# Optimization experiments

Hardware: AMD Instinct MI355X
Metric: run time of the kernel (lower is better)

The kernel has to match this reference:

```python
import jax, jax.numpy as jnp
import numpy as np

DIM = 768
HEADS = 12
HIDDEN = 4 * DIM
EPS = 1e-5


def _layer_norm(x, g, b):
    mu = jnp.mean(x, axis=-1, keepdims=True)
    var = jnp.mean(jnp.square(x - mu), axis=-1, keepdims=True)
    return (x - mu) * jax.lax.rsqrt(var + EPS) * g + b


def setup_inputs() -> dict:
    key = jax.random.key(0)
    ks = jax.random.split(key, 10)
    B, N, C = 16, 1024, DIM
    s = lambda fan: 1.0 / np.sqrt(fan)
    return {
        "x": jax.random.normal(ks[0], (B, N, C), dtype=jnp.float32),
        "ln1_g": jnp.ones((C,), jnp.float32),
        "ln1_b": jnp.zeros((C,), jnp.float32),
        "qkv_w": jax.random.normal(ks[1], (C, 3 * C), jnp.float32) * s(C),
        "qkv_b": jnp.zeros((3 * C,), jnp.float32),
        "proj_w": jax.random.normal(ks[2], (C, C), jnp.float32) * s(C),
        "proj_b": jnp.zeros((C,), jnp.float32),
        "ln2_g": jnp.ones((C,), jnp.float32),
        "ln2_b": jnp.zeros((C,), jnp.float32),
        "fc1_w": jax.random.normal(ks[3], (C, HIDDEN), jnp.float32) * s(C),
        "fc1_b": jnp.zeros((HIDDEN,), jnp.float32),
        "fc2_w": jax.random.normal(ks[4], (HIDDEN, C), jnp.float32) * s(HIDDEN),
        "fc2_b": jnp.zeros((C,), jnp.float32),
    }


def reference(x, ln1_g, ln1_b, qkv_w, qkv_b, proj_w, proj_b,
              ln2_g, ln2_b, fc1_w, fc1_b, fc2_w, fc2_b):
    B, N, C = x.shape
    Hd = C // HEADS
    scale = Hd ** -0.5

    # --- attention branch (pre-norm) ---
    h = _layer_norm(x, ln1_g, ln1_b)
    qkv = h @ qkv_w + qkv_b                       # [B,N,3C]
    qkv = qkv.reshape(B, N, 3, HEADS, Hd).transpose(2, 0, 3, 1, 4)
    q, k, v = qkv[0], qkv[1], qkv[2]              # [B,H,N,Hd]
    attn = jnp.einsum("bhqd,bhkd->bhqk", q, k) * scale
    attn = jax.nn.softmax(attn, axis=-1)
    o = jnp.einsum("bhqk,bhkd->bhqd", attn, v)    # [B,H,N,Hd]
    o = o.transpose(0, 2, 1, 3).reshape(B, N, C)
    x = x + (o @ proj_w + proj_b)

    # --- MLP branch (pre-norm) ---
    h = _layer_norm(x, ln2_g, ln2_b)
    h = jax.nn.gelu(h @ fc1_w + fc1_b, approximate=False)
    x = x + (h @ fc2_w + fc2_b)
    return x
```

## Files before the change

kernel.cpp:

```cpp
#include <hip/hip_runtime.h>

typedef __bf16 bf16x8 __attribute__((ext_vector_type(8)));
typedef __bf16 bf16x4 __attribute__((ext_vector_type(4)));
typedef float f32x4 __attribute__((ext_vector_type(4)));
typedef float f32x16 __attribute__((ext_vector_type(16)));

#define MFMA16(a,b,c) __builtin_amdgcn_mfma_f32_16x16x32_bf16((a),(b),(c),0,0,0)
#define MFMA32(a,b,c) __builtin_amdgcn_mfma_f32_32x32x16_bf16((a),(b),(c),0,0,0)
#define EXP2R(x) __builtin_amdgcn_exp2f(x)

#define BB   16
#define SEQ  1024
#define CD   768
#define NHD  12
#define HDD  64
#define HID  3072
#define MT   (BB*SEQ)

__device__ __forceinline__ void gload16(const void* g, void* l) {
    __builtin_amdgcn_global_load_lds(
        (const __attribute__((address_space(1))) void*)g,
        (__attribute__((address_space(3))) void*)l, 16, 0, 0);
}

__device__ __forceinline__ unsigned pk2(float lo, float hi) {
    unsigned short a = __builtin_bit_cast(unsigned short, (__bf16)lo);
    unsigned short b = __builtin_bit_cast(unsigned short, (__bf16)hi);
    return (unsigned)a | ((unsigned)b << 16);
}

__device__ __forceinline__ float fast_gelu(float x) {
    float u = x * x * x;
    float y = fmaf(0.044715f, u, x);
    float e = EXP2R(-2.3022083f * y);
    return x * __builtin_amdgcn_rcpf(1.0f + e);
}

__global__ __launch_bounds__(256)
void transpose_w(const float* __restrict__ W, __bf16* __restrict__ WT, int R, int C)
{
    __shared__ float t[32][33];
    int tc = C >> 5;
    int bid = blockIdx.x;
    int br = bid / tc, bc = bid % tc;
    int x = threadIdx.x & 31, y = threadIdx.x >> 5;
#pragma unroll
    for (int i = 0; i < 4; ++i)
        t[y + 8*i][x] = W[(size_t)(br*32 + y + 8*i)*C + bc*32 + x];
    __syncthreads();
#pragma unroll
    for (int i = 0; i < 4; ++i)
        WT[(size_t)(bc*32 + y + 8*i)*R + br*32 + x] = (__bf16)t[x][y + 8*i];
}

__global__ __launch_bounds__(256)
void ln_kernel(const float* __restrict__ xin, const float* __restrict__ g,
               const float* __restrict__ bb, __bf16* out)
{
    int row = blockIdx.x * 4 + (threadIdx.x >> 6);
    int lane = threadIdx.x & 63;
    const float* xr = xin + (size_t)row * CD + lane * 4;
    float4 v0 = *(const float4*)(xr);
    float4 v1 = *(const float4*)(xr + 256);
    float4 v2 = *(const float4*)(xr + 512);
    float s = v0.x+v0.y+v0.z+v0.w + v1.x+v1.y+v1.z+v1.w + v2.x+v2.y+v2.z+v2.w;
#pragma unroll
    for (int off = 1; off < 64; off <<= 1) s += __shfl_xor(s, off);
    float mu = s * (1.0f/768.0f);
    float q =
        (v0.x-mu)*(v0.x-mu)+(v0.y-mu)*(v0.y-mu)+(v0.z-mu)*(v0.z-mu)+(v0.w-mu)*(v0.w-mu)+
        (v1.x-mu)*(v1.x-mu)+(v1.y-mu)*(v1.y-mu)+(v1.z-mu)*(v1.z-mu)+(v1.w-mu)*(v1.w-mu)+
        (v2.x-mu)*(v2.x-mu)+(v2.y-mu)*(v2.y-mu)+(v2.z-mu)*(v2.z-mu)+(v2.w-mu)*(v2.w-mu);
#pragma unroll
    for (int off = 1; off < 64; off <<= 1) q += __shfl_xor(q, off);
    float rstd = rsqrtf(q * (1.0f/768.0f) + 1e-5f);

    __bf16* orow = out + (size_t)row * CD + lane * 4;
#pragma unroll
    for (int p = 0; p < 3; ++p) {
        float4 xv = (p == 0) ? v0 : (p == 1) ? v1 : v2;
        float4 gv = *(const float4*)(g  + p*256 + lane*4);
        float4 bv = *(const float4*)(bb + p*256 + lane*4);
        bf16x4 ov;
        ov[0] = (__bf16)((xv.x-mu)*rstd*gv.x + bv.x);
        ov[1] = (__bf16)((xv.y-mu)*rstd*gv.y + bv.y);
        ov[2] = (__bf16)((xv.z-mu)*rstd*gv.z + bv.z);
        ov[3] = (__bf16)((xv.w-mu)*rstd*gv.w + bv.w);
        *(bf16x4*)(orow + p*256) = ov;
    }
}

template<int EPI>
__global__ __launch_bounds__(256)
void gemm_bt(const __bf16* __restrict__ A, const __bf16* __restrict__ BT,
             const float* __restrict__ bias,
             const float* res, float* outf,
             __bf16* __restrict__ outb,
             __bf16* __restrict__ qb, __bf16* __restrict__ kb, __bf16* __restrict__ vb,
             int M, int N, int K)
{
    __shared__ alignas(16) __bf16 lsA[2][128*64];
    __shared__ alignas(16) __bf16 lsB[2][128*64];

    int nbn = N >> 7;
    int nwg = (M >> 7) * nbn;
    int bid = (int)blockIdx.x;
    int cpx = nwg >> 3;
    int sw = (bid & 7) * cpx + (bid >> 3);
    int bm = sw / nbn, bn = sw % nbn;
    int row0 = bm << 7, col0 = bn << 7;

    int tid = threadIdx.x;
    int lane = tid & 63, w = tid >> 6;
    int wr = w >> 1, wc = w & 1;
    int lr = lane & 15, lg = lane >> 4;

    f32x4 acc[4][4] = {};
    int sbase = w * 4096 + lane * 16;
    int swz = (lr & 7) << 4;

    auto stage = [&](int buf, int ktE) {
#pragma unroll
        for (int i = 0; i < 4; ++i) {
            int s = sbase + (i << 10);
            int r = s >> 7;
            int ch = ((s >> 4) & 7) ^ (r & 7);
            gload16(A  + (size_t)(row0 + r)*K + (ktE + ch*8),
                    (char*)lsA + buf*16384 + (w*4 + i)*1024);
            gload16(BT + (size_t)(col0 + r)*K + (ktE + ch*8),
                    (char*)lsB + buf*16384 + (w*4 + i)*1024);
        }
    };

    int nkt = K >> 6;
    stage(0, 0);
    __syncthreads();
    int cur = 0;

    for (int kt = 0; kt < nkt; ++kt) {
        if (kt + 1 < nkt) stage(cur ^ 1, (kt + 1) << 6);

        const char* lA = (const char*)lsA + cur*16384;
        const char* lB = (const char*)lsB + cur*16384;
#pragma unroll
        for (int ks = 0; ks < 2; ++ks) {
            int cb = (ks*64 + lg*16) ^ swz;
            bf16x8 af[4], bfv[4];
#pragma unroll
            for (int m = 0; m < 4; ++m) {
                af[m]  = *(const bf16x8*)(lA + (wr*64 + m*16 + lr)*128 + cb);
                bfv[m] = *(const bf16x8*)(lB + (wc*64 + m*16 + lr)*128 + cb);
            }
#pragma unroll
            for (int m = 0; m < 4; ++m)
#pragma unroll
                for (int n = 0; n < 4; ++n)
                    acc[m][n] = MFMA16(af[m], bfv[n], acc[m][n]);
        }
        __syncthreads();
        cur ^= 1;
    }

    int rbase = row0 + wr*64 + lg*4;
    int cbase = col0 + wc*64 + lr;
#pragma unroll
    for (int n = 0; n < 4; ++n) {
        int col = cbase + n*16;
        float bv = bias[col];
        if constexpr (EPI == 0) {
            int which = col / CD;
            int c2 = col - which * CD;
            int head = c2 >> 6, d = c2 & 63;
#pragma unroll
            for (int m = 0; m < 4; ++m) {
                int r0 = rbase + m*16;
                int b = r0 >> 10, nn = r0 & 1023;
                if (which == 2) {
                    bf16x4 pv;
#pragma unroll
                    for (int j = 0; j < 4; ++j) pv[j] = (__bf16)(acc[m][n][j] + bv);
                    *(bf16x4*)&vb[(((size_t)b*NHD + head)*HDD + d)*SEQ + nn] = pv;
                } else {
                    __bf16* dst = (which == 0) ? qb : kb;
#pragma unroll
                    for (int j = 0; j < 4; ++j)
                        dst[(((size_t)b*NHD + head)*SEQ + nn + j)*HDD + d] =
                            (__bf16)(acc[m][n][j] + bv);
                }
            }
        } else {
#pragma unroll
            for (int m = 0; m < 4; ++m) {
                int rr = rbase + m*16;
#pragma unroll
                for (int j = 0; j < 4; ++j) {
                    float val = acc[m][n][j] + bv;
                    int r = rr + j;
                    if constexpr (EPI == 1) {
                        outf[(size_t)r*N + col] = res[(size_t)r*N + col] + val;
                    } else {
                        outb[(size_t)r*N + col] = (__bf16)fast_gelu(val);
                    }
                }
            }
        }
    }
}

__global__ __launch_bounds__(256)
void attn_kernel(const __bf16* __restrict__ q, const __bf16* __restrict__ k,
                 const __bf16* __restrict__ vT, __bf16* __restrict__ o)
{
    __shared__ alignas(16) __bf16 kls[2][64*64];
    __shared__ alignas(16) __bf16 vls[2][64*64];

    int bid = blockIdx.x;
    int u = bid >> 3, x = bid & 7;
    int bh = x*24 + (u >> 3);
    int qt = u & 7;
    int b = bh / NHD, hh = bh % NHD;
    int tid = threadIdx.x, lane = tid & 63, w = tid >> 6;
    int lq = lane & 31, h = lane >> 5;

    int qg = qt*128 + w*32 + lq;
    const __bf16* qp = q + ((size_t)bh*SEQ + qg)*HDD + h*8;
    bf16x8 qf[4];
#pragma unroll
    for (int s = 0; s < 4; ++s) qf[s] = *(const bf16x8*)(qp + s*16);

    const __bf16* kbase = k  + (size_t)bh*SEQ*HDD;
    const __bf16* vbase = vT + (size_t)bh*HDD*SEQ;

    int srow0 = tid >> 3;
    int scol0 = ((tid & 7) ^ (srow0 & 7)) * 8;
    int srow1 = srow0 + 32;

    auto stage = [&](int buf, int kv) {
        char* kl = (char*)kls + buf*8192 + w*1024;
        char* vl = (char*)vls + buf*8192 + w*1024;
        gload16(kbase + (size_t)(kv + srow0)*HDD + scol0, kl);
        gload16(kbase + (size_t)(kv + srow1)*HDD + scol0, kl + 4096);
        gload16(vbase + (size_t)srow0*SEQ + kv + scol0, vl);
        gload16(vbase + (size_t)srow1*SEQ + kv + scol0, vl + 4096);
    };

    const float SCL2 = 0.125f * 1.44269504f;
    const float NB   = -12.0f * SCL2;
    float lrun = 0.f;
    f32x16 oa0 = {}, oa1 = {};

    stage(0, 0);
    __syncthreads();
    int cur = 0;
    int rswz = (lq & 7) << 4;

    for (int kt = 0; kt < SEQ/64; ++kt) {
        if (kt + 1 < SEQ/64) stage(cur ^ 1, (kt + 1)*64);

        const char* kc = (const char*)kls + cur*8192;
        const char* vc = (const char*)vls + cur*8192;

        bf16x8 ka0[4], ka1[4];
#pragma unroll
        for (int s = 0; s < 4; ++s) {
            int bc = (h*16 + s*32) ^ rswz;
            ka0[s] = *(const bf16x8*)(kc + lq*128 + bc);
            ka1[s] = *(const bf16x8*)(kc + (lq + 32)*128 + bc);
        }
        bf16x8 vf0[4], vf1[4];
#pragma unroll
        for (int g = 0; g < 4; ++g) {
            int bc = (h*16 + g*32) ^ rswz;
            vf0[g] = *(const bf16x8*)(vc + lq*128 + bc);
            vf1[g] = *(const bf16x8*)(vc + (lq + 32)*128 + bc);
        }

        f32x16 s0 = {}, s1 = {};
        __builtin_amdgcn_s_setprio(1);
#pragma unroll
        for (int s = 0; s < 4; ++s) {
            s0 = MFMA32(ka0[s], qf[s], s0);
            s1 = MFMA32(ka1[s], qf[s], s1);
        }
        __builtin_amdgcn_s_setprio(0);

#pragma unroll
        for (int i = 0; i < 16; ++i) s0[i] = EXP2R(fmaf(s0[i], SCL2, NB));
#pragma unroll
        for (int i = 0; i < 16; ++i) s1[i] = EXP2R(fmaf(s1[i], SCL2, NB));
        float a8[8];
#pragma unroll
        for (int i = 0; i < 8; ++i)
            a8[i] = (s0[i] + s0[i + 8]) + (s1[i] + s1[i + 8]);
        float s4a = (a8[0] + a8[1]) + (a8[2] + a8[3]);
        float s4b = (a8[4] + a8[5]) + (a8[6] + a8[7]);
        lrun += s4a + s4b;

#pragma unroll
        for (int t = 0; t < 2; ++t) {
            const f32x16& sp = t ? s1 : s0;
            unsigned d0 = pk2(sp[ 0], sp[ 1]);
            unsigned d1 = pk2(sp[ 2], sp[ 3]);
            unsigned d2 = pk2(sp[ 4], sp[ 5]);
            unsigned d3 = pk2(sp[ 6], sp[ 7]);
            unsigned d4 = pk2(sp[ 8], sp[ 9]);
            unsigned d5 = pk2(sp[10], sp[11]);
            unsigned d6 = pk2(sp[12], sp[13]);
            unsigned d7 = pk2(sp[14], sp[15]);
            unsigned pd0 = __shfl_xor(d0, 32), pd1 = __shfl_xor(d1, 32);
            unsigned pd2 = __shfl_xor(d2, 32), pd3 = __shfl_xor(d3, 32);
            unsigned pd4 = __shfl_xor(d4, 32), pd5 = __shfl_xor(d5, 32);
            unsigned pd6 = __shfl_xor(d6, 32), pd7 = __shfl_xor(d7, 32);
            union { unsigned u[4]; bf16x8 v; } f0, f1;
            f0.u[0] = h ? pd2 : d0;
            f0.u[1] = h ? pd3 : d1;
            f0.u[2] = h ? d2 : pd0;
            f0.u[3] = h ? d3 : pd1;
            f1.u[0] = h ? pd6 : d4;
            f1.u[1] = h ? pd7 : d5;
            f1.u[2] = h ? d6 : pd4;
            f1.u[3] = h ? d7 : pd5;
            __builtin_amdgcn_s_setprio(1);
            oa0 = MFMA32(vf0[t*2 + 0], f0.v, oa0);
            oa1 = MFMA32(vf1[t*2 + 0], f0.v, oa1);
            oa0 = MFMA32(vf0[t*2 + 1], f1.v, oa0);
            oa1 = MFMA32(vf1[t*2 + 1], f1.v, oa1);
            __builtin_amdgcn_s_setprio(0);
        }

        __syncthreads();
        cur ^= 1;
    }

    lrun += __shfl_xor(lrun, 32);
    float inv = __builtin_amdgcn_rcpf(lrun);
    oa0 = oa0 * inv;
    oa1 = oa1 * inv;
    __bf16* orow = o + ((size_t)b*SEQ + qg)*CD + hh*HDD;
#pragma unroll
    for (int dt = 0; dt < 2; ++dt) {
        f32x16 oa = dt ? oa1 : oa0;
        unsigned d0 = pk2(oa[ 0], oa[ 1]);
        unsigned d1 = pk2(oa[ 2], oa[ 3]);
        unsigned d2 = pk2(oa[ 4], oa[ 5]);
        unsigned d3 = pk2(oa[ 6], oa[ 7]);
        unsigned d4 = pk2(oa[ 8], oa[ 9]);
        unsigned d5 = pk2(oa[10], oa[11]);
        unsigned d6 = pk2(oa[12], oa[13]);
        unsigned d7 = pk2(oa[14], oa[15]);
        unsigned pd0 = __shfl_xor(d0, 32), pd1 = __shfl_xor(d1, 32);
        unsigned pd2 = __shfl_xor(d2, 32), pd3 = __shfl_xor(d3, 32);
        unsigned pd4 = __shfl_xor(d4, 32), pd5 = __shfl_xor(d5, 32);
        unsigned pd6 = __shfl_xor(d6, 32), pd7 = __shfl_xor(d7, 32);
        union { unsigned u[4]; bf16x8 v; } g0, g1;
        g0.u[0] = h ? pd2 : d0;
        g0.u[1] = h ? pd3 : d1;
        g0.u[2] = h ? d2 : pd0;
        g0.u[3] = h ? d3 : pd1;
        g1.u[0] = h ? pd6 : d4;
        g1.u[1] = h ? pd7 : d5;
        g1.u[2] = h ? d6 : pd4;
        g1.u[3] = h ? d7 : pd5;
        *(bf16x8*)(orow + dt*32 +  0 + h*8) = g0.v;
        *(bf16x8*)(orow + dt*32 + 16 + h*8) = g1.v;
    }
}

extern "C" void kernel_launch(void* const* d_in, const int* in_sizes, int n_in,
                              void* d_out, int out_size, void* d_ws, size_t ws_size,
                              hipStream_t stream)
{
    const float* x     = (const float*)d_in[0];
    const float* ln1g  = (const float*)d_in[1];
    const float* ln1b  = (const float*)d_in[2];
    const float* qkvw  = (const float*)d_in[3];
    const float* qkvb  = (const float*)d_in[4];
    const float* projw = (const float*)d_in[5];
    const float* projb = (const float*)d_in[6];
    const float* ln2g  = (const float*)d_in[7];
    const float* ln2b  = (const float*)d_in[8];
    const float* fc1w  = (const float*)d_in[9];
    const float* fc1b  = (const float*)d_in[10];
    const float* fc2w  = (const float*)d_in[11];
    const float* fc2b  = (const float*)d_in[12];
    float* out = (float*)d_out;

    char* p = (char*)d_ws;
    auto alloc = [&](size_t bytes) { char* r = p; p += (bytes + 255) & ~(size_t)255; return r; };
    __bf16* wqkvT  = (__bf16*)alloc((size_t)3*CD*CD*2);
    __bf16* wprojT = (__bf16*)alloc((size_t)CD*CD*2);
    __bf16* wfc1T  = (__bf16*)alloc((size_t)HID*CD*2);
    __bf16* wfc2T  = (__bf16*)alloc((size_t)CD*HID*2);
    __bf16* hbuf   = (__bf16*)alloc((size_t)MT*CD*2);
    __bf16* qbuf   = (__bf16*)alloc((size_t)BB*NHD*SEQ*HDD*2);
    __bf16* kbuf   = (__bf16*)alloc((size_t)BB*NHD*SEQ*HDD*2);
    __bf16* vtbuf  = (__bf16*)alloc((size_t)BB*NHD*SEQ*HDD*2);
    (void)alloc((size_t)BB*NHD*SEQ*HDD*2);
    __bf16* hhbuf  = qbuf;

    transpose_w<<<(CD/32)*(3*CD/32), 256, 0, stream>>>(qkvw,  wqkvT, CD, 3*CD);
    transpose_w<<<(CD/32)*(CD/32),   256, 0, stream>>>(projw, wprojT, CD, CD);
    transpose_w<<<(CD/32)*(HID/32),  256, 0, stream>>>(fc1w,  wfc1T, CD, HID);
    transpose_w<<<(HID/32)*(CD/32),  256, 0, stream>>>(fc2w,  wfc2T, HID, CD);

    ln_kernel<<<MT/4, 256, 0, stream>>>(x, ln1g, ln1b, hbuf);

    gemm_bt<0><<<(MT/128)*(3*CD/128), 256, 0, stream>>>(
        hbuf, wqkvT, qkvb, nullptr, nullptr, nullptr, qbuf, kbuf, vtbuf, MT, 3*CD, CD);

    attn_kernel<<<BB*NHD*8, 256, 0, stream>>>(qbuf, kbuf, vtbuf, hbuf);

    gemm_bt<1><<<(MT/128)*(CD/128), 256, 0, stream>>>(
        hbuf, wprojT, projb, x, out, nullptr, nullptr, nullptr, nullptr, MT, CD, CD);

    ln_kernel<<<MT/4, 256, 0, stream>>>(out, ln2g, ln2b, hbuf);

    gemm_bt<2><<<(MT/128)*(HID/128), 256, 0, stream>>>(
        hbuf, wfc1T, fc1b, nullptr, nullptr, hhbuf, nullptr, nullptr, nullptr, MT, HID, CD);

    gemm_bt<1><<<(MT/128)*(CD/128), 256, 0, stream>>>(
        hhbuf, wfc2T, fc2b, out, out, nullptr, nullptr, nullptr, nullptr, MT, CD, HID);
}
```

Before: 463.5 us.

## Load GEMM B operand directly to registers and fuse prep kernels into one launch

The GEMM no longer stages the B (weight) tile through LDS. Each wave loads its B fragments straight from global memory into registers, which halves LDS use and allows a launch bound of 3 blocks per CU. The sync scheme becomes raw s_barrier with a manual vmcnt wait. Separately, the four weight transposes and the first layernorm are merged into one prep kernel launch to cut launch overhead. The risks are uncoalesced or redundant global B loads across waves, more register pressure, and fragile hand-written waitcnt counts.

```diff
diff --git a/kernel.cpp b/kernel.cpp
--- a/kernel.cpp
+++ b/kernel.cpp
@@ -8,6 +8,7 @@
 #define MFMA16(a,b,c) __builtin_amdgcn_mfma_f32_16x16x32_bf16((a),(b),(c),0,0,0)
 #define MFMA32(a,b,c) __builtin_amdgcn_mfma_f32_32x32x16_bf16((a),(b),(c),0,0,0)
 #define EXP2R(x) __builtin_amdgcn_exp2f(x)
+#define SBAR() asm volatile("s_barrier" ::: "memory")
 
 #define BB   16
 #define SEQ  1024
@@ -36,12 +37,11 @@
     return x * __builtin_amdgcn_rcpf(1.0f + e);
 }
 
-__global__ __launch_bounds__(256)
-void transpose_w(const float* __restrict__ W, __bf16* __restrict__ WT, int R, int C)
-{
-    __shared__ float t[32][33];
+__device__ __forceinline__ void transpose_body(
+    const float* __restrict__ W, __bf16* __restrict__ WT, int R, int C, int bid,
+    float (*t)[33])
+{
     int tc = C >> 5;
-    int bid = blockIdx.x;
     int br = bid / tc, bc = bid % tc;
     int x = threadIdx.x & 31, y = threadIdx.x >> 5;
 #pragma unroll
@@ -53,11 +53,11 @@
         WT[(size_t)(bc*32 + y + 8*i)*R + br*32 + x] = (__bf16)t[x][y + 8*i];
 }
 
-__global__ __launch_bounds__(256)
-void ln_kernel(const float* __restrict__ xin, const float* __restrict__ g,
-               const float* __restrict__ bb, __bf16* out)
-{
-    int row = blockIdx.x * 4 + (threadIdx.x >> 6);
+__device__ __forceinline__ void ln_body(
+    const float* __restrict__ xin, const float* __restrict__ g,
+    const float* __restrict__ bb, __bf16* out, int bid)
+{
+    int row = bid * 4 + ((int)threadIdx.x >> 6);
     int lane = threadIdx.x & 63;
     const float* xr = xin + (size_t)row * CD + lane * 4;
     float4 v0 = *(const float4*)(xr);
@@ -90,8 +90,33 @@
     }
 }
 
+__global__ __launch_bounds__(256)
+void prep_kernel(const float* qkvw, const float* projw, const float* fc1w, const float* fc2w,
+                 __bf16* wqkvT, __bf16* wprojT, __bf16* wfc1T, __bf16* wfc2T,
+                 const float* x, const float* g1, const float* b1, __bf16* hbuf)
+{
+    __shared__ float t[32][33];
+    int bid = blockIdx.x;
+    if (bid < 1728) { transpose_body(qkvw,  wqkvT,  CD,  3*CD, bid, t); return; }
+    bid -= 1728;
+    if (bid < 576)  { transpose_body(projw, wprojT, CD,  CD,   bid, t); return; }
+    bid -= 576;
+    if (bid < 2304) { transpose_body(fc1w,  wfc1T,  CD,  HID,  bid, t); return; }
+    bid -= 2304;
+    if (bid < 2304) { transpose_body(fc2w,  wfc2T,  HID, CD,   bid, t); return; }
+    bid -= 2304;
+    ln_body(x, g1, b1, hbuf, bid);
+}
+
+__global__ __launch_bounds__(256)
+void ln_kernel(const float* __restrict__ xin, const float* __restrict__ g,
+               const float* __restrict__ bb, __bf16* out)
+{
+    ln_body(xin, g, bb, out, blockIdx.x);
+}
+
 template<int EPI>
-__global__ __launch_bounds__(256)
+__global__ __launch_bounds__(256, 3)
 void gemm_bt(const __bf16* __restrict__ A, const __bf16* __restrict__ BT,
              const float* __restrict__ bias,
              const float* res, float* outf,
@@ -100,7 +125,6 @@
              int M, int N, int K)
 {
     __shared__ alignas(16) __bf16 lsA[2][128*64];
-    __shared__ alignas(16) __bf16 lsB[2][128*64];
 
     int nbn = N >> 7;
     int nwg = (M >> 7) * nbn;
@@ -119,46 +143,53 @@
     int sbase = w * 4096 + lane * 16;
     int swz = (lr & 7) << 4;
 
-    auto stage = [&](int buf, int ktE) {
+    auto stageA = [&](int buf, int ktE) {
 #pragma unroll
         for (int i = 0; i < 4; ++i) {
             int s = sbase + (i << 10);
             int r = s >> 7;
             int ch = ((s >> 4) & 7) ^ (r & 7);
-            gload16(A  + (size_t)(row0 + r)*K + (ktE + ch*8),
+            gload16(A + (size_t)(row0 + r)*K + (ktE + ch*8),
                     (char*)lsA + buf*16384 + (w*4 + i)*1024);
-            gload16(BT + (size_t)(col0 + r)*K + (ktE + ch*8),
-                    (char*)lsB + buf*16384 + (w*4 + i)*1024);
         }
     };
 
+    const __bf16* bp = BT + (size_t)(col0 + wc*64 + lr)*K + lg*8;
+
     int nkt = K >> 6;
-    stage(0, 0);
-    __syncthreads();
-    int cur = 0;
+    stageA(0, 0);
 
     for (int kt = 0; kt < nkt; ++kt) {
-        if (kt + 1 < nkt) stage(cur ^ 1, (kt + 1) << 6);
+        int cur = kt & 1;
+        if (kt) SBAR();
+
+        int ke = kt << 6;
+        bf16x8 bfr[2][4];
+#pragma unroll
+        for (int n = 0; n < 4; ++n)
+#pragma unroll
+            for (int ks = 0; ks < 2; ++ks)
+                bfr[ks][n] = *(const bf16x8*)(bp + (size_t)n*16*K + ke + ks*32);
+        __builtin_amdgcn_sched_barrier(0);
+
+        if (kt + 1 < nkt) stageA(cur ^ 1, (kt + 1) << 6);
+        asm volatile("s_waitcnt vmcnt(12)" ::: "memory");
+        SBAR();
 
         const char* lA = (const char*)lsA + cur*16384;
-        const char* lB = (const char*)lsB + cur*16384;
 #pragma unroll
         for (int ks = 0; ks < 2; ++ks) {
             int cb = (ks*64 + lg*16) ^ swz;
-            bf16x8 af[4], bfv[4];
-#pragma unroll
-            for (int m = 0; m < 4; ++m) {
-                af[m]  = *(const bf16x8*)(lA + (wr*64 + m*16 + lr)*128 + cb);
-                bfv[m] = *(const bf16x8*)(lB + (wc*64 + m*16 + lr)*128 + cb);
-            }
+            bf16x8 af[4];
 #pragma unroll
             for (int m = 0; m < 4; ++m)
+                af[m] = *(const bf16x8*)(lA + (wr*64 + m*16 + lr)*128 + cb);
+#pragma unroll
+            for (int m = 0; m < 4; ++m)
 #pragma unroll
                 for (int n = 0; n < 4; ++n)
-                    acc[m][n] = MFMA16(af[m], bfv[n], acc[m][n]);
-        }
-        __syncthreads();
-        cur ^= 1;
+                    acc[m][n] = MFMA16(af[m], bfr[ks][n], acc[m][n]);
+        }
     }
 
     int rbase = row0 + wr*64 + lg*4;
@@ -398,12 +429,8 @@
     (void)alloc((size_t)BB*NHD*SEQ*HDD*2);
     __bf16* hhbuf  = qbuf;
 
-    transpose_w<<<(CD/32)*(3*CD/32), 256, 0, stream>>>(qkvw,  wqkvT, CD, 3*CD);
-    transpose_w<<<(CD/32)*(CD/32),   256, 0, stream>>>(projw, wprojT, CD, CD);
-    transpose_w<<<(CD/32)*(HID/32),  256, 0, stream>>>(fc1w,  wfc1T, CD, HID);
-    transpose_w<<<(HID/32)*(CD/32),  256, 0, stream>>>(fc2w,  wfc2T, HID, CD);
-
-    ln_kernel<<<MT/4, 256, 0, stream>>>(x, ln1g, ln1b, hbuf);
+    prep_kernel<<<1728 + 576 + 2304 + 2304 + MT/4, 256, 0, stream>>>(
+        qkvw, projw, fc1w, fc2w, wqkvT, wprojT, wfc1T, wfc2T, x, ln1g, ln1b, hbuf);
 
     gemm_bt<0><<<(MT/128)*(3*CD/128), 256, 0, stream>>>(
         hbuf, wqkvT, qkvb, nullptr, nullptr, nullptr, qbuf, kbuf, vtbuf, MT, 3*CD, CD);
```

After: 660.4 us. +42.5%, slower.
